# Performance work log

Measured on AMD Instinct MI355X. Metric: run time of the kernel, lower is better.

Reference implementation:

```python
import jax, jax.numpy as jnp
import numpy as np

EPS = 1e-5

def setup_inputs() -> dict:
    key = jax.random.key(0)
    ks = jax.random.split(key, 12)
    B = 4096
    x = jax.random.normal(ks[0], (B, 28, 28, 1), dtype=jnp.float32)
    # BatchNorm1d(1) affine params (applied per-channel over active sites)
    bn_gamma = jnp.ones((1,), jnp.float32)
    bn_beta = jnp.zeros((1,), jnp.float32)
    # SubMConv2d weights, HWIO layout
    w1 = jax.random.normal(ks[1], (3, 3, 1, 32), jnp.float32) * 0.1
    b1 = jax.random.normal(ks[2], (32,), jnp.float32) * 0.01
    w2 = jax.random.normal(ks[3], (3, 3, 32, 64), jnp.float32) * 0.05
    b2 = jax.random.normal(ks[4], (64,), jnp.float32) * 0.01
    # FC layers (torch Linear: y = x @ W.T + b)
    fcw1 = jax.random.normal(ks[5], (128, 14 * 14 * 64), jnp.float32) * 0.01
    fcb1 = jnp.zeros((128,), jnp.float32)
    fcw2 = jax.random.normal(ks[6], (10, 128), jnp.float32) * 0.05
    fcb2 = jnp.zeros((10,), jnp.float32)
    return {"x": x, "bn_gamma": bn_gamma, "bn_beta": bn_beta,
            "w1": w1, "b1": b1, "w2": w2, "b2": b2,
            "fcw1": fcw1, "fcb1": fcb1, "fcw2": fcw2, "fcb2": fcb2}

def _subm_conv(feat, mask, w, b):
    # Submanifold conv: inactive inputs are zero (already masked), and the
    # output coordinate set equals the input active set -> mask the output.
    y = jax.lax.conv_general_dilated(
        feat, w, window_strides=(1, 1), padding='SAME',
        dimension_numbers=('NHWC', 'HWIO', 'NHWC'))
    return jnp.where(mask, y + b, 0.0)

def reference(x, bn_gamma, bn_beta, w1, b1, w2, b2, fcw1, fcb1, fcw2, fcb2):
    # from_dense: active sites are locations with nonzero feature. [B,28,28,1]
    mask = (x != 0)  # single channel -> site mask [B,28,28,1]
    maskf = mask.astype(x.dtype)
    # BatchNorm1d(1) on the [N_active, 1] sparse feature tensor (batch stats)
    n = jnp.maximum(maskf.sum(), 1.0)
    mean = (x * maskf).sum() / n
    var = (jnp.square(x - mean) * maskf).sum() / n
    feat = maskf * (bn_gamma * (x - mean) * jax.lax.rsqrt(var + EPS) + bn_beta)
    # SubMConv2d(1,32,3,1) + ReLU
    h = jax.nn.relu(_subm_conv(feat, mask, w1, b1))  # [B,28,28,32]
    # SubMConv2d(32,64,3,1) + ReLU
    h = jax.nn.relu(_subm_conv(h, mask, w2, b2))     # [B,28,28,64]
    # SparseMaxPool2d(2,2): max over active sites per window; since values are
    # post-ReLU (>=0) and inactive sites hold 0, dense maxpool is exact, and
    # fully-inactive windows correctly yield 0 after ToDense.
    h = jax.lax.reduce_window(h, -jnp.inf, jax.lax.max,
                              (1, 2, 2, 1), (1, 2, 2, 1), 'VALID')  # [B,14,14,64]
    # ToDense gives NCHW [B,64,14,14]; torch.flatten uses C-major order
    h = jnp.transpose(h, (0, 3, 1, 2)).reshape(h.shape[0], -1)  # [B,12544]
    # dropout1/dropout2 are identity in eval mode
    h = jax.nn.relu(h @ fcw1.T + fcb1)
    logits = h @ fcw2.T + fcb2
    return jax.nn.log_softmax(logits, axis=1)
```

## Files before the change

kernel.cpp:

```cpp
#include <hip/hip_runtime.h>
#include <stdint.h>

typedef unsigned short u16;
typedef unsigned int u32;
typedef __attribute__((ext_vector_type(8))) short bf16x8;
typedef __attribute__((ext_vector_type(4))) float f32x4;

__device__ __forceinline__ u16 f2bf(float f) {
    u32 u = __float_as_uint(f);
    u32 r = (u + 0x7fffu + ((u >> 16) & 1u)) >> 16;
    return (u16)r;
}

__device__ __forceinline__ void gload16(const u16* src, u16* dst) {
    __builtin_amdgcn_global_load_lds(
        (const __attribute__((address_space(1))) u32*)src,
        (__attribute__((address_space(3))) u32*)dst, 16, 0, 0);
}

__global__ __launch_bounds__(256) void k_stats(const float* __restrict__ x, int n,
                                               float* __restrict__ stats) {
    int t = blockIdx.x * 256 + threadIdx.x;
    int stride = gridDim.x * 256;
    float c = 0.f, s = 0.f, ss = 0.f;
    for (int i = t; i < n; i += stride) {
        float v = x[i];
        if (v != 0.f) { c += 1.f; s += v; ss = fmaf(v, v, ss); }
    }
    for (int off = 32; off > 0; off >>= 1) {
        c  += __shfl_down(c, off);
        s  += __shfl_down(s, off);
        ss += __shfl_down(ss, off);
    }
    __shared__ float red[3][4];
    int lane = threadIdx.x & 63, wv = threadIdx.x >> 6;
    if (lane == 0) { red[0][wv] = c; red[1][wv] = s; red[2][wv] = ss; }
    __syncthreads();
    if (threadIdx.x == 0) {
        atomicAdd(&stats[0], red[0][0] + red[0][1] + red[0][2] + red[0][3]);
        atomicAdd(&stats[1], red[1][0] + red[1][1] + red[1][2] + red[1][3]);
        atomicAdd(&stats[2], red[2][0] + red[2][1] + red[2][2] + red[2][3]);
    }
}

__global__ void k_finalize(const float* __restrict__ g, const float* __restrict__ b,
                           float* __restrict__ stats) {
    float n = stats[0]; if (n < 1.f) n = 1.f;
    float mean = stats[1] / n;
    float var = stats[2] / n - mean * mean;
    if (var < 0.f) var = 0.f;
    float scale = g[0] * rsqrtf(var + 1e-5f);
    stats[4] = scale;
    stats[5] = b[0] - mean * scale;
}

__global__ __launch_bounds__(256) void k_prep(const float* __restrict__ w2,
                                              u16* __restrict__ w2b) {
    int i = blockIdx.x * 256 + threadIdx.x;
    if (i < 9 * 64 * 32) {
        int tap = i >> 11, rem = i & 2047, co = rem >> 5, ci = rem & 31;
        w2b[i] = f2bf(w2[tap * 2048 + ci * 64 + co]);
    }
}

__global__ __launch_bounds__(256) void k_prepw(const float* __restrict__ fcw1,
                                               u16* __restrict__ fcw1b, int n) {
    int i = blockIdx.x * 256 + threadIdx.x;
    if (i < n) fcw1b[i] = f2bf(fcw1[i]);
}

__global__ __launch_bounds__(256, 2) void k_conv(const float* __restrict__ x,
    const float* __restrict__ w1, const float* __restrict__ b1,
    const u16* __restrict__ w2b, const float* __restrict__ b2,
    const float* __restrict__ stats, u16* __restrict__ pooled)
{
    __shared__ u16 h1[28800];
    __shared__ float feat[30][30];
    __shared__ unsigned char mk[784];
    const int t = threadIdx.x;
    const int b = blockIdx.x;
    const int lane = t & 63;
    const int wv = t >> 6;
    const int lg = lane >> 4;
    const int lr = lane & 15;

    bf16x8 wf[9][4];
    #pragma unroll
    for (int tap = 0; tap < 9; ++tap)
        #pragma unroll
        for (int nt = 0; nt < 4; ++nt)
            wf[tap][nt] = *(const bf16x8*)(w2b + tap * 2048 + (nt * 16 + lr) * 32 + lg * 8);
    float bias2[4];
    #pragma unroll
    for (int nt = 0; nt < 4; ++nt) bias2[nt] = b2[nt * 16 + lr];

    const float scale = stats[4], shift = stats[5];

    for (int i = t; i < 14400; i += 256) ((u32*)h1)[i] = 0u;
    for (int i = t; i < 900; i += 256) (&feat[0][0])[i] = 0.f;
    __syncthreads();

    const float* xb = x + (size_t)b * 784;
    for (int i = t; i < 784; i += 256) {
        float v = xb[i];
        bool m = (v != 0.f);
        mk[i] = m ? 1 : 0;
        int h = i / 28, w = i - h * 28;
        feat[h + 1][w + 1] = m ? fmaf(v, scale, shift) : 0.f;
    }
    __syncthreads();

    {
        const int cp = t & 15, pxg = t >> 4;
        float wk0[9], wk1[9];
        const float bs0 = b1[2 * cp], bs1 = b1[2 * cp + 1];
        #pragma unroll
        for (int j = 0; j < 9; ++j) {
            wk0[j] = w1[j * 32 + 2 * cp];
            wk1[j] = w1[j * 32 + 2 * cp + 1];
        }
        const int hslot = (cp >> 2) * 7200 + (cp & 3) * 2;
        for (int px = pxg; px < 784; px += 16) {
            if (!mk[px]) continue;
            int h = px / 28, w = px - h * 28;
            float a0 = bs0, a1 = bs1;
            #pragma unroll
            for (int kh = 0; kh < 3; ++kh)
                #pragma unroll
                for (int kw = 0; kw < 3; ++kw) {
                    float f = feat[h + kh][w + kw];
                    a0 = fmaf(f, wk0[kh * 3 + kw], a0);
                    a1 = fmaf(f, wk1[kh * 3 + kw], a1);
                }
            u32 pk = (u32)f2bf(fmaxf(a0, 0.f)) | ((u32)f2bf(fmaxf(a1, 0.f)) << 16);
            *(u32*)&h1[hslot + ((h + 1) * 30 + (w + 1)) * 8] = pk;
        }
    }
    __syncthreads();

    const int win = lr >> 2, dyl = (lr >> 1) & 1, dxl = lr & 1;
    const f32x4 zero4 = {0.f, 0.f, 0.f, 0.f};
    for (int mt = wv; mt < 56; mt += 4) {
        const int r = mt >> 2, cg = mt & 3;
        const int ih = 2 * r + dyl;
        int iw = 2 * (cg * 4 + win) + dxl;
        if (iw > 27) iw = 27;
        const char* abase = (const char*)h1 + lg * 14400 + (ih * 30 + iw) * 16;

        f32x4 acc[4];
        #pragma unroll
        for (int nt = 0; nt < 4; ++nt) acc[nt] = zero4;

        #pragma unroll
        for (int tap = 0; tap < 9; ++tap) {
            const int kh = tap / 3, kw = tap - kh * 3;
            bf16x8 af = *(const bf16x8*)(abase + (kh * 30 + kw) * 16);
            #pragma unroll
            for (int nt = 0; nt < 4; ++nt)
                acc[nt] = __builtin_amdgcn_mfma_f32_16x16x32_bf16(af, wf[tap][nt], acc[nt], 0, 0, 0);
        }

        const int pc = cg * 4 + lg;
        if (pc < 14) {
            const int m00 = mk[(2 * r) * 28 + 2 * pc];
            const int m01 = mk[(2 * r) * 28 + 2 * pc + 1];
            const int m10 = mk[(2 * r + 1) * 28 + 2 * pc];
            const int m11 = mk[(2 * r + 1) * 28 + 2 * pc + 1];
            #pragma unroll
            for (int nt = 0; nt < 4; ++nt) {
                float v0 = m00 ? fmaxf(acc[nt][0] + bias2[nt], 0.f) : 0.f;
                float v1 = m01 ? fmaxf(acc[nt][1] + bias2[nt], 0.f) : 0.f;
                float v2 = m10 ? fmaxf(acc[nt][2] + bias2[nt], 0.f) : 0.f;
                float v3 = m11 ? fmaxf(acc[nt][3] + bias2[nt], 0.f) : 0.f;
                float best = fmaxf(fmaxf(v0, v1), fmaxf(v2, v3));
                pooled[(size_t)b * 12544 + (nt * 16 + lr) * 196 + r * 14 + pc] = f2bf(best);
            }
        }
    }
}

__global__ __launch_bounds__(256, 4) void k_fc1(const u16* __restrict__ pooled,
    const u16* __restrict__ fcw1b, float* __restrict__ fc1, int M)
{
    __shared__ u16 Asm[8 * 64 * 8];
    __shared__ u16 Bsm[8 * 128 * 8];
    const int t = threadIdx.x;
    const int m0 = blockIdx.x * 64;
    const int kbase = blockIdx.y * 896;
    const int lane = t & 63;
    const int wv = t >> 6;
    const int lg = lane >> 4, lr = lane & 15;
    const int wm = wv & 1, wn = wv >> 1;

    const int ia0 = t, ia1 = t + 256;
    const u16* as0 = pooled + (size_t)(m0 + (ia0 & 63)) * 12544 + (ia0 >> 6) * 8 + kbase;
    const u16* as1 = pooled + (size_t)(m0 + (ia1 & 63)) * 12544 + (ia1 >> 6) * 8 + kbase;
    const u16* bs0 = fcw1b + (size_t)(t & 127) * 12544 + ((t >> 7) + 0) * 8 + kbase;
    const u16* bs1 = fcw1b + (size_t)(t & 127) * 12544 + ((t >> 7) + 2) * 8 + kbase;
    const u16* bs2 = fcw1b + (size_t)(t & 127) * 12544 + ((t >> 7) + 4) * 8 + kbase;
    const u16* bs3 = fcw1b + (size_t)(t & 127) * 12544 + ((t >> 7) + 6) * 8 + kbase;
    u16* ad0 = &Asm[(size_t)ia0 * 8];
    u16* ad1 = &Asm[(size_t)ia1 * 8];
    u16* bd0 = &Bsm[(size_t)(t + 0) * 8];
    u16* bd1 = &Bsm[(size_t)(t + 256) * 8];
    u16* bd2 = &Bsm[(size_t)(t + 512) * 8];
    u16* bd3 = &Bsm[(size_t)(t + 768) * 8];

    f32x4 acc[2][4];
    #pragma unroll
    for (int mi = 0; mi < 2; ++mi)
        #pragma unroll
        for (int ni = 0; ni < 4; ++ni) acc[mi][ni] = (f32x4){0.f, 0.f, 0.f, 0.f};

    for (int s = 0; s < 14; ++s) {
        const int kk = s * 64;
        __syncthreads();
        gload16(as0 + kk, ad0);
        gload16(as1 + kk, ad1);
        gload16(bs0 + kk, bd0);
        gload16(bs1 + kk, bd1);
        gload16(bs2 + kk, bd2);
        gload16(bs3 + kk, bd3);
        asm volatile("s_waitcnt vmcnt(0)" ::: "memory");
        __syncthreads();
        #pragma unroll
        for (int ks = 0; ks < 2; ++ks) {
            bf16x8 a[2], bfr[4];
            #pragma unroll
            for (int mi = 0; mi < 2; ++mi)
                a[mi] = *(const bf16x8*)&Asm[(((ks * 4 + lg) * 64) + wm * 32 + mi * 16 + lr) * 8];
            #pragma unroll
            for (int ni = 0; ni < 4; ++ni)
                bfr[ni] = *(const bf16x8*)&Bsm[(((ks * 4 + lg) * 128) + wn * 64 + ni * 16 + lr) * 8];
            #pragma unroll
            for (int mi = 0; mi < 2; ++mi)
                #pragma unroll
                for (int ni = 0; ni < 4; ++ni)
                    acc[mi][ni] = __builtin_amdgcn_mfma_f32_16x16x32_bf16(a[mi], bfr[ni], acc[mi][ni], 0, 0, 0);
        }
    }

    #pragma unroll
    for (int mi = 0; mi < 2; ++mi)
        #pragma unroll
        for (int ni = 0; ni < 4; ++ni)
            #pragma unroll
            for (int q = 0; q < 4; ++q) {
                int m = m0 + wm * 32 + mi * 16 + lg * 4 + q;
                int n = wn * 64 + ni * 16 + lr;
                atomicAdd(&fc1[(size_t)m * 128 + n], acc[mi][ni][q]);
            }
}

__global__ __launch_bounds__(256) void k_fc2(const float* __restrict__ fc1,
    const float* __restrict__ fcb1, const float* __restrict__ fcw2,
    const float* __restrict__ fcb2, float* __restrict__ out, int M)
{
    __shared__ float red[4][64][10];
    const int t = threadIdx.x;
    const int ml = t & 63, kq = t >> 6;
    const int m = blockIdx.x * 64 + ml;
    float acc[10];
    #pragma unroll
    for (int c = 0; c < 10; ++c) acc[c] = 0.f;
    const float* fp = fc1 + (size_t)m * 128 + kq * 32;
    #pragma unroll 2
    for (int j = 0; j < 32; j += 4) {
        float4 v4 = *(const float4*)(fp + j);
        float vv[4] = {v4.x, v4.y, v4.z, v4.w};
        #pragma unroll
        for (int u = 0; u < 4; ++u) {
            int k = kq * 32 + j + u;
            float v = fmaxf(vv[u] + fcb1[k], 0.f);
            #pragma unroll
            for (int c = 0; c < 10; ++c) acc[c] = fmaf(v, fcw2[c * 128 + k], acc[c]);
        }
    }
    #pragma unroll
    for (int c = 0; c < 10; ++c) red[kq][ml][c] = acc[c];
    __syncthreads();
    if (kq == 0) {
        float lgt[10];
        #pragma unroll
        for (int c = 0; c < 10; ++c)
            lgt[c] = red[0][ml][c] + red[1][ml][c] + red[2][ml][c] + red[3][ml][c] + fcb2[c];
        float mx = lgt[0];
        #pragma unroll
        for (int c = 1; c < 10; ++c) mx = fmaxf(mx, lgt[c]);
        float se = 0.f;
        #pragma unroll
        for (int c = 0; c < 10; ++c) se += expf(lgt[c] - mx);
        float lse = mx + logf(se);
        #pragma unroll
        for (int c = 0; c < 10; ++c) out[(size_t)m * 10 + c] = lgt[c] - lse;
    }
}

extern "C" void kernel_launch(void* const* d_in, const int* in_sizes, int n_in,
                              void* d_out, int out_size, void* d_ws, size_t ws_size,
                              hipStream_t stream) {
    const float* x     = (const float*)d_in[0];
    const float* gamma = (const float*)d_in[1];
    const float* beta  = (const float*)d_in[2];
    const float* w1    = (const float*)d_in[3];
    const float* b1    = (const float*)d_in[4];
    const float* w2    = (const float*)d_in[5];
    const float* b2    = (const float*)d_in[6];
    const float* fcw1  = (const float*)d_in[7];
    const float* fcb1  = (const float*)d_in[8];
    const float* fcw2  = (const float*)d_in[9];
    const float* fcb2  = (const float*)d_in[10];
    float* out = (float*)d_out;

    const int B = in_sizes[0] / 784;

    float* stats  = (float*)d_ws;
    u16*   w2b    = (u16*)((char*)d_ws + 256);
    float* fc1    = (float*)((char*)d_ws + 256);
    u16*   pooled = (u16*)((char*)d_ws + 256 + (size_t)B * 128 * 4);
    u16*   fcw1b  = (u16*)((char*)d_ws + 256 + (size_t)B * 128 * 4 + (size_t)B * 12544 * 2);

    hipMemsetAsync(stats, 0, 32, stream);
    k_stats<<<1024, 256, 0, stream>>>(x, B * 784, stats);
    k_finalize<<<1, 1, 0, stream>>>(gamma, beta, stats);
    k_prep<<<72, 256, 0, stream>>>(w2, w2b);
    k_prepw<<<(128 * 12544 + 255) / 256, 256, 0, stream>>>(fcw1, fcw1b, 128 * 12544);
    k_conv<<<B, 256, 0, stream>>>(x, w1, b1, w2b, b2, stats, pooled);
    hipMemsetAsync(fc1, 0, (size_t)B * 128 * 4, stream);
    k_fc1<<<dim3(B / 64, 14), 256, 0, stream>>>(pooled, fcw1b, fc1, B);
    k_fc2<<<B / 64, 256, 0, stream>>>(fc1, fcb1, fcw2, fcb2, out, B);
}
```

Measured before the change: 399.7 us.

## Widen conv kernel to 512 threads, split output channels across waves, merge prep kernels

The conv kernel now runs 512 threads per image. Each wave handles two of the four 16-channel output groups and one column group across all rows, which halves per-wave weight registers and targets higher occupancy. Conv1 computes four channels per thread with 8-byte LDS stores. A precomputed 2x2 pool mask byte replaces four mask loads, and the bias is folded into the accumulator init. The two weight-conversion kernels are merged into one launch. The risk is LDS-bound occupancy (about 60KB per block) limiting the gain from more threads.

```diff
diff --git a/kernel.cpp b/kernel.cpp
--- a/kernel.cpp
+++ b/kernel.cpp
@@ -54,22 +54,18 @@
     stats[5] = b[0] - mean * scale;
 }
 
-__global__ __launch_bounds__(256) void k_prep(const float* __restrict__ w2,
-                                              u16* __restrict__ w2b) {
+__global__ __launch_bounds__(256) void k_prepall(const float* __restrict__ w2,
+    const float* __restrict__ fcw1, u16* __restrict__ w2b, u16* __restrict__ fcw1b, int n)
+{
     int i = blockIdx.x * 256 + threadIdx.x;
     if (i < 9 * 64 * 32) {
         int tap = i >> 11, rem = i & 2047, co = rem >> 5, ci = rem & 31;
         w2b[i] = f2bf(w2[tap * 2048 + ci * 64 + co]);
     }
-}
-
-__global__ __launch_bounds__(256) void k_prepw(const float* __restrict__ fcw1,
-                                               u16* __restrict__ fcw1b, int n) {
-    int i = blockIdx.x * 256 + threadIdx.x;
     if (i < n) fcw1b[i] = f2bf(fcw1[i]);
 }
 
-__global__ __launch_bounds__(256, 2) void k_conv(const float* __restrict__ x,
+__global__ __launch_bounds__(512, 4) void k_conv(const float* __restrict__ x,
     const float* __restrict__ w1, const float* __restrict__ b1,
     const u16* __restrict__ w2b, const float* __restrict__ b2,
     const float* __restrict__ stats, u16* __restrict__ pooled)
@@ -77,31 +73,34 @@
     __shared__ u16 h1[28800];
     __shared__ float feat[30][30];
     __shared__ unsigned char mk[784];
+    __shared__ unsigned char pm[196];
     const int t = threadIdx.x;
     const int b = blockIdx.x;
     const int lane = t & 63;
     const int wv = t >> 6;
     const int lg = lane >> 4;
     const int lr = lane & 15;
-
-    bf16x8 wf[9][4];
+    const int wn2 = wv & 1;
+    const int wq = wv >> 1;
+
+    bf16x8 wf[9][2];
     #pragma unroll
     for (int tap = 0; tap < 9; ++tap)
         #pragma unroll
-        for (int nt = 0; nt < 4; ++nt)
-            wf[tap][nt] = *(const bf16x8*)(w2b + tap * 2048 + (nt * 16 + lr) * 32 + lg * 8);
-    float bias2[4];
-    #pragma unroll
-    for (int nt = 0; nt < 4; ++nt) bias2[nt] = b2[nt * 16 + lr];
+        for (int j = 0; j < 2; ++j)
+            wf[tap][j] = *(const bf16x8*)(w2b + tap * 2048 + ((wn2 * 2 + j) * 16 + lr) * 32 + lg * 8);
+    float bias2[2];
+    #pragma unroll
+    for (int j = 0; j < 2; ++j) bias2[j] = b2[(wn2 * 2 + j) * 16 + lr];
 
     const float scale = stats[4], shift = stats[5];
 
-    for (int i = t; i < 14400; i += 256) ((u32*)h1)[i] = 0u;
-    for (int i = t; i < 900; i += 256) (&feat[0][0])[i] = 0.f;
+    for (int i = t; i < 14400; i += 512) ((u32*)h1)[i] = 0u;
+    for (int i = t; i < 900; i += 512) (&feat[0][0])[i] = 0.f;
     __syncthreads();
 
     const float* xb = x + (size_t)b * 784;
-    for (int i = t; i < 784; i += 256) {
+    for (int i = t; i < 784; i += 512) {
         float v = xb[i];
         bool m = (v != 0.f);
         mk[i] = m ? 1 : 0;
@@ -110,70 +109,85 @@
     }
     __syncthreads();
 
+    if (t < 196) {
+        int rr = t / 14, cc = t - rr * 14;
+        int base = rr * 56 + cc * 2;
+        pm[t] = (unsigned char)(mk[base] | (mk[base + 1] << 1)
+              | (mk[base + 28] << 2) | (mk[base + 29] << 3));
+    }
+
     {
-        const int cp = t & 15, pxg = t >> 4;
-        float wk0[9], wk1[9];
-        const float bs0 = b1[2 * cp], bs1 = b1[2 * cp + 1];
-        #pragma unroll
-        for (int j = 0; j < 9; ++j) {
-            wk0[j] = w1[j * 32 + 2 * cp];
-            wk1[j] = w1[j * 32 + 2 * cp + 1];
-        }
-        const int hslot = (cp >> 2) * 7200 + (cp & 3) * 2;
-        for (int px = pxg; px < 784; px += 16) {
+        const int cp = t & 7, pxg = t >> 3;
+        float wk[9][4];
+        float bs[4];
+        #pragma unroll
+        for (int c = 0; c < 4; ++c) bs[c] = b1[cp * 4 + c];
+        #pragma unroll
+        for (int j = 0; j < 9; ++j)
+            #pragma unroll
+            for (int c = 0; c < 4; ++c) wk[j][c] = w1[j * 32 + cp * 4 + c];
+        u16* hb = h1 + (cp >> 1) * 7200 + (cp & 1) * 4;
+        for (int px = pxg; px < 784; px += 64) {
             if (!mk[px]) continue;
             int h = px / 28, w = px - h * 28;
-            float a0 = bs0, a1 = bs1;
+            float a0 = bs[0], a1 = bs[1], a2 = bs[2], a3 = bs[3];
             #pragma unroll
             for (int kh = 0; kh < 3; ++kh)
                 #pragma unroll
                 for (int kw = 0; kw < 3; ++kw) {
                     float f = feat[h + kh][w + kw];
-                    a0 = fmaf(f, wk0[kh * 3 + kw], a0);
-                    a1 = fmaf(f, wk1[kh * 3 + kw], a1);
+                    a0 = fmaf(f, wk[kh * 3 + kw][0], a0);
+                    a1 = fmaf(f, wk[kh * 3 + kw][1], a1);
+                    a2 = fmaf(f, wk[kh * 3 + kw][2], a2);
+                    a3 = fmaf(f, wk[kh * 3 + kw][3], a3);
                 }
-            u32 pk = (u32)f2bf(fmaxf(a0, 0.f)) | ((u32)f2bf(fmaxf(a1, 0.f)) << 16);
-            *(u32*)&h1[hslot + ((h + 1) * 30 + (w + 1)) * 8] = pk;
+            u32 lo = (u32)f2bf(fmaxf(a0, 0.f)) | ((u32)f2bf(fmaxf(a1, 0.f)) << 16);
+            u32 hi = (u32)f2bf(fmaxf(a2, 0.f)) | ((u32)f2bf(fmaxf(a3, 0.f)) << 16);
+            *(uint2*)&hb[((h + 1) * 30 + (w + 1)) * 8] = make_uint2(lo, hi);
         }
     }
     __syncthreads();
 
     const int win = lr >> 2, dyl = (lr >> 1) & 1, dxl = lr & 1;
-    const f32x4 zero4 = {0.f, 0.f, 0.f, 0.f};
-    for (int mt = wv; mt < 56; mt += 4) {
-        const int r = mt >> 2, cg = mt & 3;
+    int iw = 2 * (wq * 4 + win) + dxl;
+    if (iw > 27) iw = 27;
+    const int pc = wq * 4 + lg;
+    u16* poolb = pooled + (size_t)b * 12544;
+    for (int r = 0; r < 14; ++r) {
         const int ih = 2 * r + dyl;
-        int iw = 2 * (cg * 4 + win) + dxl;
-        if (iw > 27) iw = 27;
         const char* abase = (const char*)h1 + lg * 14400 + (ih * 30 + iw) * 16;
 
-        f32x4 acc[4];
-        #pragma unroll
-        for (int nt = 0; nt < 4; ++nt) acc[nt] = zero4;
-
+        f32x4 acc0 = {bias2[0], bias2[0], bias2[0], bias2[0]};
+        f32x4 acc1 = {bias2[1], bias2[1], bias2[1], bias2[1]};
         #pragma unroll
         for (int tap = 0; tap < 9; ++tap) {
             const int kh = tap / 3, kw = tap - kh * 3;
             bf16x8 af = *(const bf16x8*)(abase + (kh * 30 + kw) * 16);
-            #pragma unroll
-            for (int nt = 0; nt < 4; ++nt)
-                acc[nt] = __builtin_amdgcn_mfma_f32_16x16x32_bf16(af, wf[tap][nt], acc[nt], 0, 0, 0);
-        }
-
-        const int pc = cg * 4 + lg;
+            acc0 = __builtin_amdgcn_mfma_f32_16x16x32_bf16(af, wf[tap][0], acc0, 0, 0, 0);
+            acc1 = __builtin_amdgcn_mfma_f32_16x16x32_bf16(af, wf[tap][1], acc1, 0, 0, 0);
+        }
+
         if (pc < 14) {
-            const int m00 = mk[(2 * r) * 28 + 2 * pc];
-            const int m01 = mk[(2 * r) * 28 + 2 * pc + 1];
-            const int m10 = mk[(2 * r + 1) * 28 + 2 * pc];
-            const int m11 = mk[(2 * r + 1) * 28 + 2 * pc + 1];
-            #pragma unroll
-            for (int nt = 0; nt < 4; ++nt) {
-                float v0 = m00 ? fmaxf(acc[nt][0] + bias2[nt], 0.f) : 0.f;
-                float v1 = m01 ? fmaxf(acc[nt][1] + bias2[nt], 0.f) : 0.f;
-                float v2 = m10 ? fmaxf(acc[nt][2] + bias2[nt], 0.f) : 0.f;
-                float v3 = m11 ? fmaxf(acc[nt][3] + bias2[nt], 0.f) : 0.f;
+            int pmv = pm[r * 14 + pc];
+            float mf0 = (pmv & 1) ? 1.f : 0.f;
+            float mf1 = (pmv & 2) ? 1.f : 0.f;
+            float mf2 = (pmv & 4) ? 1.f : 0.f;
+            float mf3 = (pmv & 8) ? 1.f : 0.f;
+            {
+                float v0 = fmaxf(acc0[0], 0.f) * mf0;
+                float v1 = fmaxf(acc0[1], 0.f) * mf1;
+                float v2 = fmaxf(acc0[2], 0.f) * mf2;
+                float v3 = fmaxf(acc0[3], 0.f) * mf3;
                 float best = fmaxf(fmaxf(v0, v1), fmaxf(v2, v3));
-                pooled[(size_t)b * 12544 + (nt * 16 + lr) * 196 + r * 14 + pc] = f2bf(best);
+                poolb[((wn2 * 2 + 0) * 16 + lr) * 196 + r * 14 + pc] = f2bf(best);
+            }
+            {
+                float v0 = fmaxf(acc1[0], 0.f) * mf0;
+                float v1 = fmaxf(acc1[1], 0.f) * mf1;
+                float v2 = fmaxf(acc1[2], 0.f) * mf2;
+                float v3 = fmaxf(acc1[3], 0.f) * mf3;
+                float best = fmaxf(fmaxf(v0, v1), fmaxf(v2, v3));
+                poolb[((wn2 * 2 + 1) * 16 + lr) * 196 + r * 14 + pc] = f2bf(best);
             }
         }
     }
@@ -323,9 +337,8 @@
     hipMemsetAsync(stats, 0, 32, stream);
     k_stats<<<1024, 256, 0, stream>>>(x, B * 784, stats);
     k_finalize<<<1, 1, 0, stream>>>(gamma, beta, stats);
-    k_prep<<<72, 256, 0, stream>>>(w2, w2b);
-    k_prepw<<<(128 * 12544 + 255) / 256, 256, 0, stream>>>(fcw1, fcw1b, 128 * 12544);
-    k_conv<<<B, 256, 0, stream>>>(x, w1, b1, w2b, b2, stats, pooled);
+    k_prepall<<<(128 * 12544 + 255) / 256, 256, 0, stream>>>(w2, fcw1, w2b, fcw1b, 128 * 12544);
+    k_conv<<<B, 512, 0, stream>>>(x, w1, b1, w2b, b2, stats, pooled);
     hipMemsetAsync(fc1, 0, (size_t)B * 128 * 4, stream);
     k_fc1<<<dim3(B / 64, 14), 256, 0, stream>>>(pooled, fcw1b, fc1, B);
     k_fc2<<<B / 64, 256, 0, stream>>>(fc1, fcb1, fcw2, fcb2, out, B);
```

After: 390.4 us. 2.3% less time.
